# Kernel tuning notes

Hardware: AMD Instinct MI355X
Metric: run time of the kernel (lower is better)

## Reference

```python
import jax, jax.numpy as jnp
import numpy as np

B, A, E = 16384, 8, 512


def setup_inputs() -> dict:
    key = jax.random.key(0)
    ks = jax.random.split(key, 6)
    return {
        "image_features": jax.random.normal(ks[0], (B, E), dtype=jnp.float32),
        "edge_attributes": jax.random.normal(ks[1], (B, A, E), dtype=jnp.float32),
        "linear_w": jax.random.normal(ks[2], (E, 2 * E), dtype=jnp.float32) * (1.0 / np.sqrt(2 * E)),
        "linear_b": jax.random.normal(ks[3], (E,), dtype=jnp.float32) * 0.01,
        "fwd_proj": jax.random.normal(ks[4], (A, E, E), dtype=jnp.float32) * (1.0 / np.sqrt(E)),
        "bwd_proj": jax.random.normal(ks[5], (A, E, E), dtype=jnp.float32) * (1.0 / np.sqrt(E)),
        "self_weighted": jnp.ones((1, A, 1), dtype=jnp.float32),
    }


def reference(image_features, edge_attributes, linear_w, linear_b, fwd_proj, bwd_proj, self_weighted):
    # Forward attribute GNN: broadcast src over attribute axis, concat, linear(2E->E)
    src = jnp.broadcast_to(image_features[:, None, :], edge_attributes.shape)  # [B,A,E]
    x = jnp.concatenate([src, edge_attributes], axis=-1)                       # [B,A,2E]
    agg = jnp.einsum('bak,ek->bae', x, linear_w) + linear_b                    # [B,A,E]
    attr_rep = jnp.einsum('bai,aij->baj', agg, fwd_proj)                       # [B,A,E]

    # Backward attribute GNN: per-type projection, ReLU, learned weighted sum over A
    proj = jnp.einsum('bai,aij->baj', attr_rep, bwd_proj)                      # [B,A,E]
    individuals = jnp.sum(jax.nn.relu(proj) * self_weighted, axis=1)           # [B,E]
    return attr_rep, individuals
```

## Files before the change

kernel.cpp:

```cpp
#include <hip/hip_runtime.h>
#include <cstdint>
#include <cstddef>

#define NB 16384
#define NA 8
#define NE 512
#define NK 1024
#define NN 4096

typedef __bf16 bf16x8 __attribute__((ext_vector_type(8)));
typedef float  f32x4  __attribute__((ext_vector_type(4)));
typedef uint16_t u16x8 __attribute__((ext_vector_type(8)));

__device__ __forceinline__ uint16_t cvt_bf16(float f) {
    uint32_t u = __builtin_bit_cast(uint32_t, f);
    u += 0x7fffu + ((u >> 16) & 1u);
    return (uint16_t)(u >> 16);
}

__device__ __forceinline__ int swz(int row) { return (row ^ (row >> 2)) & 3; }

__device__ __forceinline__ int cf_pos(int row, int c) {
    return ((row >> 1) << 3) + ((((row & 1) << 2) + c) ^ ((row >> 1) & 7));
}

__device__ __forceinline__ void gl_lds16(const void* g, void* l) {
    __builtin_amdgcn_global_load_lds(
        (__attribute__((address_space(1))) void*)(void*)g,
        (__attribute__((address_space(3))) void*)l, 16, 0, 0);
}

__device__ __forceinline__ void tcvt_tile(const float* __restrict__ src,
                                          uint16_t* __restrict__ dst,
                                          int R, int C, int c0, int r0, int t) {
    __shared__ float tile[32][33];
    int tx = t & 31, ty = t >> 5;
#pragma unroll
    for (int yy = 0; yy < 4; ++yy) {
        int r = ty + yy * 8;
        tile[r][tx] = src[(size_t)(r0 + r) * C + c0 + tx];
    }
    __syncthreads();
#pragma unroll
    for (int yy = 0; yy < 4; ++yy) {
        int c = ty + yy * 8;
        dst[(size_t)(c0 + c) * R + r0 + tx] = cvt_bf16(tile[tx][c]);
    }
}

__global__ __launch_bounds__(256) void k_pre(const float* __restrict__ lw,
                                             const float* __restrict__ fwd,
                                             const float* __restrict__ bwd,
                                             const float* __restrict__ img,
                                             const float* __restrict__ lb,
                                             uint16_t* __restrict__ lwT,
                                             uint16_t* __restrict__ fwdT,
                                             uint16_t* __restrict__ bwdT,
                                             uint16_t* __restrict__ imgb,
                                             float* __restrict__ bvec) {
    int b = blockIdx.x, t = threadIdx.x;
    if (b < 512) {
        int bx = b & 31, by = b >> 5;
        tcvt_tile(lw, lwT, NE, NK, bx * 32, by * 32, t);
    } else if (b < 2560) {
        int i = b - 512;
        int mat = i >> 8, bx = i & 15, by = (i >> 4) & 15;
        tcvt_tile(fwd + (size_t)mat * NE * NE, fwdT + (size_t)mat * NE * NE,
                  NE, NE, bx * 32, by * 32, t);
    } else if (b < 4608) {
        int i = b - 2560;
        int mat = i >> 8, bx = i & 15, by = (i >> 4) & 15;
        tcvt_tile(bwd + (size_t)mat * NE * NE, bwdT + (size_t)mat * NE * NE,
                  NE, NE, bx * 32, by * 32, t);
    } else if (b < 12800) {
        int i = (b - 4608) * 256 + t;
        float4 v = ((const float4*)img)[i];
        ushort4 o;
        o.x = cvt_bf16(v.x); o.y = cvt_bf16(v.y); o.z = cvt_bf16(v.z); o.w = cvt_bf16(v.w);
        ((ushort4*)imgb)[i] = o;
    } else {
        int i = b - 12800;
        int a = i >> 4, i0 = (i & 15) * 32;
        float s0 = 0.f, s1 = 0.f;
#pragma unroll 4
        for (int k = 0; k < 32; ++k) {
            float w = lb[i0 + k];
            const float* f = fwd + ((size_t)a * NE + i0 + k) * NE;
            s0 = fmaf(w, f[t], s0);
            s1 = fmaf(w, f[t + 256], s1);
        }
        atomicAdd(&bvec[a * NE + t], s0);
        atomicAdd(&bvec[a * NE + t + 256], s1);
    }
}

__global__ __launch_bounds__(256) void k_prep(const uint16_t* __restrict__ lwT,
                                              const uint16_t* __restrict__ fwdT,
                                              uint16_t* __restrict__ TMT) {
    __shared__ alignas(16) uint16_t lA[128 * 32];
    __shared__ alignas(16) uint16_t lB[128 * 32];
    int bz = blockIdx.x;
    int nt = bz & 31, mt = bz >> 5;
    int m0 = mt * 128, n0 = nt * 128;
    int t = threadIdx.x, lane = t & 63;
    int w = t >> 6, wm = w >> 1, wn = w & 1;
    int lr = lane & 15, lc = lane >> 4;
    int sl = swz(lr);
    f32x4 acc[4][4] = {};
    for (int k0 = 0; k0 < NE; k0 += 32) {
        __syncthreads();
#pragma unroll
        for (int p = 0; p < 2; ++p) {
            int idx = p * 256 + t;
            int row = idx >> 2, c16 = (idx & 3) ^ swz(row);
            gl_lds16(lwT + (size_t)(m0 + row) * NE + k0 + c16 * 8, lA + idx * 8);
            gl_lds16(fwdT + (size_t)(n0 + row) * NE + k0 + c16 * 8, lB + idx * 8);
        }
        __syncthreads();
        bf16x8 af[4], bfr[4];
#pragma unroll
        for (int i = 0; i < 4; ++i)
            af[i] = *(const bf16x8*)&lA[(wm * 64 + i * 16 + lr) * 32 + ((lc ^ sl) << 3)];
#pragma unroll
        for (int j = 0; j < 4; ++j)
            bfr[j] = *(const bf16x8*)&lB[(wn * 64 + j * 16 + lr) * 32 + ((lc ^ sl) << 3)];
#pragma unroll
        for (int i = 0; i < 4; ++i)
#pragma unroll
            for (int j = 0; j < 4; ++j)
                acc[i][j] = __builtin_amdgcn_mfma_f32_16x16x32_bf16(af[i], bfr[j], acc[i][j], 0, 0, 0);
    }
#pragma unroll
    for (int i = 0; i < 4; ++i) {
        int mb = m0 + wm * 64 + i * 16 + lc * 4;
#pragma unroll
        for (int j = 0; j < 4; ++j) {
            int n = n0 + wn * 64 + j * 16 + lr;
            ushort4 v;
            v.x = cvt_bf16(acc[i][j][0]);
            v.y = cvt_bf16(acc[i][j][1]);
            v.z = cvt_bf16(acc[i][j][2]);
            v.w = cvt_bf16(acc[i][j][3]);
            *(ushort4*)&TMT[(size_t)n * NK + mb] = v;
        }
    }
}

__global__ __launch_bounds__(512) void k_mm4(const uint16_t* __restrict__ imgb,
                                             const float* __restrict__ edge,
                                             const uint16_t* __restrict__ TMT,
                                             const float* __restrict__ bvec,
                                             float* __restrict__ attr) {
    __shared__ alignas(16) uint16_t lA[2][128 * 32];
    __shared__ alignas(16) uint16_t lB[2][256 * 32];
    int o = blockIdx.x;
    int a = o & 7, idx = o >> 3;
    int jt = idx & 1, mt = idx >> 1;
    int m0 = mt * 128, jb = jt * 256;
    int t = threadIdx.x, lane = t & 63;
    int w = t >> 6, wm = w >> 2, wn = w & 3;
    int lr = lane & 15, lc = lane >> 4;
    int rpA = t >> 3, qA = (t & 7) ^ (rpA & 7);
    int srA = (rpA << 1) | (qA >> 2), scA = (qA & 3) << 3;
    int srB[2], scB[2];
#pragma unroll
    for (int p = 0; p < 2; ++p) {
        int u = t + p * 512;
        int rp = u >> 3, q = (u & 7) ^ (rp & 7);
        srB[p] = (rp << 1) | (q >> 2);
        scB[p] = (q & 3) << 3;
    }
    int er = t >> 2, ec = t & 3;
    int epos = cf_pos(er, ec) * 8;
    int aoff[4], boff[4];
#pragma unroll
    for (int i = 0; i < 4; ++i) {
        aoff[i] = cf_pos(wm * 64 + i * 16 + lr, lc) * 8;
        boff[i] = cf_pos(wn * 64 + i * 16 + lr, lc) * 8;
    }
    auto stage_img = [&](int buf, int s) {
        gl_lds16(imgb + (size_t)(m0 + srA) * NE + s * 32 + scA, &lA[buf][t * 8]);
    };
    auto stage_tmt = [&](int buf, int s) {
#pragma unroll
        for (int p = 0; p < 2; ++p)
            gl_lds16(TMT + (size_t)(a * NE + jb + srB[p]) * NK + s * 32 + scB[p],
                     &lB[buf][(t + p * 512) * 8]);
    };
    f32x4 acc[4][4] = {};
    stage_img(0, 0);
    stage_tmt(0, 0);
    for (int s = 0; s < 32; ++s) {
        int cur = s & 1, nb = cur ^ 1;
        __syncthreads();
        float4 e0, e1;
        bool eN = (s < 31) && (s + 1 >= 16);
        if (s < 31) {
            if (s + 1 < 16) {
                stage_img(nb, s + 1);
            } else {
                int kk = (s + 1 - 16) * 32;
                const float* sp = edge + ((size_t)(m0 + er) * NA + a) * NE + kk + ec * 8;
                e0 = ((const float4*)sp)[0];
                e1 = ((const float4*)sp)[1];
            }
            stage_tmt(nb, s + 1);
        }
        bf16x8 af[4], bfr[4];
#pragma unroll
        for (int i = 0; i < 4; ++i) af[i] = *(const bf16x8*)&lA[cur][aoff[i]];
#pragma unroll
        for (int j = 0; j < 4; ++j) bfr[j] = *(const bf16x8*)&lB[cur][boff[j]];
#pragma unroll
        for (int i = 0; i < 4; ++i)
#pragma unroll
            for (int j = 0; j < 4; ++j)
                acc[i][j] = __builtin_amdgcn_mfma_f32_16x16x32_bf16(af[i], bfr[j], acc[i][j], 0, 0, 0);
        if (eN) {
            u16x8 ov = {cvt_bf16(e0.x), cvt_bf16(e0.y), cvt_bf16(e0.z), cvt_bf16(e0.w),
                        cvt_bf16(e1.x), cvt_bf16(e1.y), cvt_bf16(e1.z), cvt_bf16(e1.w)};
            *(u16x8*)&lA[nb][epos] = ov;
        }
    }
#pragma unroll
    for (int j = 0; j < 4; ++j) {
        float bv = bvec[a * NE + jb + wn * 64 + j * 16 + lr];
#pragma unroll
        for (int i = 0; i < 4; ++i)
#pragma unroll
            for (int r = 0; r < 4; ++r)
                acc[i][j][r] += bv;
    }
#pragma unroll
    for (int i = 0; i < 4; ++i) {
#pragma unroll
        for (int r = 0; r < 4; ++r) {
            int bm = m0 + wm * 64 + i * 16 + lc * 4 + r;
            float* orow = attr + ((size_t)bm * NA + a) * NE + jb;
#pragma unroll
            for (int j = 0; j < 4; ++j)
                orow[wn * 64 + j * 16 + lr] = acc[i][j][r];
        }
    }
}

__global__ __launch_bounds__(256) void k_ind4(const float* __restrict__ attrf,
                                              const uint16_t* __restrict__ bwdT,
                                              const float* __restrict__ sw,
                                              float* __restrict__ ind) {
    __shared__ alignas(16) uint16_t lA[2][128 * 32];
    __shared__ alignas(16) uint16_t lB[2][128 * 32];
    int o = blockIdx.x;
    int xcd = o & 7, mt = o >> 3;
    int jt = xcd >> 1, ah = xcd & 1;
    int m0 = mt * 128, jb = jt * 128, a0 = ah * 4;
    int t = threadIdx.x, lane = t & 63;
    int w = t >> 6, wm = w >> 1, wn = w & 1;
    int lr = lane & 15, lc = lane >> 4;
    int srow[2], sc8[2];
#pragma unroll
    for (int p = 0; p < 2; ++p) {
        int u = p * 256 + t;
        int rp = u >> 3, q = (u & 7) ^ (rp & 7);
        srow[p] = (rp << 1) | (q >> 2);
        sc8[p] = (q & 3) << 3;
    }
    int erow[2], ec[2], epos[2];
#pragma unroll
    for (int p = 0; p < 2; ++p) {
        int u = p * 256 + t;
        erow[p] = u >> 2; ec[p] = u & 3;
        epos[p] = cf_pos(erow[p], ec[p]) * 8;
    }
    int aoff[4], boff[4];
#pragma unroll
    for (int i = 0; i < 4; ++i) {
        aoff[i] = cf_pos(wm * 64 + i * 16 + lr, lc) * 8;
        boff[i] = cf_pos(wn * 64 + i * 16 + lr, lc) * 8;
    }
    auto stage = [&](int buf, int s) {
        int aa = a0 + (s >> 4), kk = (s & 15) * 32;
#pragma unroll
        for (int p = 0; p < 2; ++p) {
            const float* sp = attrf + ((size_t)(m0 + erow[p]) * NA + aa) * NE + kk + ec[p] * 8;
            float4 v0 = ((const float4*)sp)[0];
            float4 v1 = ((const float4*)sp)[1];
            u16x8 ov = {cvt_bf16(v0.x), cvt_bf16(v0.y), cvt_bf16(v0.z), cvt_bf16(v0.w),
                        cvt_bf16(v1.x), cvt_bf16(v1.y), cvt_bf16(v1.z), cvt_bf16(v1.w)};
            *(u16x8*)&lA[buf][epos[p]] = ov;
        }
#pragma unroll
        for (int p = 0; p < 2; ++p)
            gl_lds16(bwdT + (size_t)(aa * NE + jb + srow[p]) * NE + kk + sc8[p],
                     &lB[buf][(p * 256 + t) * 8]);
    };
    f32x4 res[4][4] = {};
    f32x4 acc[4][4] = {};
    stage(0, 0);
    for (int s = 0; s < 64; ++s) {
        int cur = s & 1;
        __syncthreads();
        if (s < 63) stage(cur ^ 1, s + 1);
        bf16x8 af[4], bfr[4];
#pragma unroll
        for (int i = 0; i < 4; ++i) af[i] = *(const bf16x8*)&lA[cur][aoff[i]];
#pragma unroll
        for (int j = 0; j < 4; ++j) bfr[j] = *(const bf16x8*)&lB[cur][boff[j]];
#pragma unroll
        for (int i = 0; i < 4; ++i)
#pragma unroll
            for (int j = 0; j < 4; ++j)
                acc[i][j] = __builtin_amdgcn_mfma_f32_16x16x32_bf16(af[i], bfr[j], acc[i][j], 0, 0, 0);
        if ((s & 15) == 15) {
            float wa = sw[a0 + (s >> 4)];
#pragma unroll
            for (int i = 0; i < 4; ++i)
#pragma unroll
                for (int j = 0; j < 4; ++j) {
#pragma unroll
                    for (int r = 0; r < 4; ++r)
                        res[i][j][r] += wa * fmaxf(acc[i][j][r], 0.f);
                    acc[i][j] = (f32x4){0.f, 0.f, 0.f, 0.f};
                }
        }
    }
#pragma unroll
    for (int i = 0; i < 4; ++i) {
#pragma unroll
        for (int r = 0; r < 4; ++r) {
            int bm = m0 + wm * 64 + i * 16 + lc * 4 + r;
            float* orow = ind + (size_t)bm * NE + jb;
#pragma unroll
            for (int j = 0; j < 4; ++j)
                atomicAdd(&orow[wn * 64 + j * 16 + lr], res[i][j][r]);
        }
    }
}

extern "C" void kernel_launch(void* const* d_in, const int* in_sizes, int n_in,
                              void* d_out, int out_size, void* d_ws, size_t ws_size,
                              hipStream_t stream) {
    (void)in_sizes; (void)n_in; (void)out_size; (void)ws_size;
    const float* img  = (const float*)d_in[0];
    const float* edge = (const float*)d_in[1];
    const float* lw   = (const float*)d_in[2];
    const float* lb   = (const float*)d_in[3];
    const float* fwd  = (const float*)d_in[4];
    const float* bwd  = (const float*)d_in[5];
    const float* sw   = (const float*)d_in[6];
    float* attr = (float*)d_out;
    float* ind  = attr + (size_t)NB * NA * NE;

    char* ws = (char*)d_ws;
    size_t off = 0;
    auto alloc = [&](size_t bytes) { void* p = ws + off; off += bytes; return p; };
    uint16_t* lwT  = (uint16_t*)alloc((size_t)NK * NE * 2);
    uint16_t* fwdT = (uint16_t*)alloc((size_t)NA * NE * NE * 2);
    uint16_t* bwdT = (uint16_t*)alloc((size_t)NA * NE * NE * 2);
    uint16_t* TMT  = (uint16_t*)alloc((size_t)NN * NK * 2);
    uint16_t* imgb = (uint16_t*)alloc((size_t)NB * NE * 2);
    float*    bvec = (float*)alloc((size_t)NN * 4);

    hipMemsetAsync(bvec, 0, (size_t)NN * 4, stream);
    hipMemsetAsync(ind, 0, (size_t)NB * NE * 4, stream);

    k_pre<<<12928, 256, 0, stream>>>(lw, fwd, bwd, img, lb, lwT, fwdT, bwdT, imgb, bvec);
    k_prep<<<(NK / 128) * (NN / 128), 256, 0, stream>>>(lwT, fwdT, TMT);

    int mm_grid = 8 * 2 * (NB / 128);
    int ind_grid = (NB / 128) * (NE / 128) * 2;

    k_mm4<<<mm_grid, 512, 0, stream>>>(imgb, edge, TMT, bvec, attr);
    k_ind4<<<ind_grid, 256, 0, stream>>>(attr, bwdT, sw, ind);
}
```

Before: 500.3 us.

## Emit bf16 copy of attr_rep and enlarge individuals kernel tiles to 128x256

```diff
diff --git a/kernel.cpp b/kernel.cpp
--- a/kernel.cpp
+++ b/kernel.cpp
@@ -146,11 +146,13 @@
     }
 }
 
+template<bool WB>
 __global__ __launch_bounds__(512) void k_mm4(const uint16_t* __restrict__ imgb,
                                              const float* __restrict__ edge,
                                              const uint16_t* __restrict__ TMT,
                                              const float* __restrict__ bvec,
-                                             float* __restrict__ attr) {
+                                             float* __restrict__ attr,
+                                             uint16_t* __restrict__ attrb) {
     __shared__ alignas(16) uint16_t lA[2][128 * 32];
     __shared__ alignas(16) uint16_t lB[2][256 * 32];
     int o = blockIdx.x;
@@ -240,38 +242,42 @@
 #pragma unroll
             for (int j = 0; j < 4; ++j)
                 orow[wn * 64 + j * 16 + lr] = acc[i][j][r];
-        }
-    }
-}
-
-__global__ __launch_bounds__(256) void k_ind4(const float* __restrict__ attrf,
+            if (WB) {
+                uint16_t* brw = attrb + ((size_t)bm * NA + a) * NE + jb;
+#pragma unroll
+                for (int j = 0; j < 4; ++j)
+                    brw[wn * 64 + j * 16 + lr] = cvt_bf16(acc[i][j][r]);
+            }
+        }
+    }
+}
+
+template<bool AB>
+__global__ __launch_bounds__(512) void k_ind5(const float* __restrict__ attrf,
+                                              const uint16_t* __restrict__ attrb,
                                               const uint16_t* __restrict__ bwdT,
                                               const float* __restrict__ sw,
                                               float* __restrict__ ind) {
     __shared__ alignas(16) uint16_t lA[2][128 * 32];
-    __shared__ alignas(16) uint16_t lB[2][128 * 32];
+    __shared__ alignas(16) uint16_t lB[2][256 * 32];
     int o = blockIdx.x;
-    int xcd = o & 7, mt = o >> 3;
-    int jt = xcd >> 1, ah = xcd & 1;
-    int m0 = mt * 128, jb = jt * 128, a0 = ah * 4;
+    int ah = o & 1, jt = (o >> 1) & 1, mt = o >> 2;
+    int m0 = mt * 128, jb = jt * 256, a0 = ah * 4;
     int t = threadIdx.x, lane = t & 63;
-    int w = t >> 6, wm = w >> 1, wn = w & 1;
+    int w = t >> 6, wm = w >> 2, wn = w & 3;
     int lr = lane & 15, lc = lane >> 4;
-    int srow[2], sc8[2];
+    int rpA = t >> 3, qA = (t & 7) ^ (rpA & 7);
+    int srA = (rpA << 1) | (qA >> 2), scA = (qA & 3) << 3;
+    int srB[2], scB[2];
 #pragma unroll
     for (int p = 0; p < 2; ++p) {
-        int u = p * 256 + t;
+        int u = t + p * 512;
         int rp = u >> 3, q = (u & 7) ^ (rp & 7);
-        srow[p] = (rp << 1) | (q >> 2);
-        sc8[p] = (q & 3) << 3;
-    }
-    int erow[2], ec[2], epos[2];
-#pragma unroll
-    for (int p = 0; p < 2; ++p) {
-        int u = p * 256 + t;
-        erow[p] = u >> 2; ec[p] = u & 3;
-        epos[p] = cf_pos(erow[p], ec[p]) * 8;
-    }
+        srB[p] = (rp << 1) | (q >> 2);
+        scB[p] = (q & 3) << 3;
+    }
+    int er = t >> 2, ec = t & 3;
+    int epos = cf_pos(er, ec) * 8;
     int aoff[4], boff[4];
 #pragma unroll
     for (int i = 0; i < 4; ++i) {
@@ -280,19 +286,21 @@
     }
     auto stage = [&](int buf, int s) {
         int aa = a0 + (s >> 4), kk = (s & 15) * 32;
-#pragma unroll
-        for (int p = 0; p < 2; ++p) {
-            const float* sp = attrf + ((size_t)(m0 + erow[p]) * NA + aa) * NE + kk + ec[p] * 8;
+        if (AB) {
+            gl_lds16(attrb + ((size_t)(m0 + srA) * NA + aa) * NE + kk + scA,
+                     &lA[buf][t * 8]);
+        } else {
+            const float* sp = attrf + ((size_t)(m0 + er) * NA + aa) * NE + kk + ec * 8;
             float4 v0 = ((const float4*)sp)[0];
             float4 v1 = ((const float4*)sp)[1];
             u16x8 ov = {cvt_bf16(v0.x), cvt_bf16(v0.y), cvt_bf16(v0.z), cvt_bf16(v0.w),
                         cvt_bf16(v1.x), cvt_bf16(v1.y), cvt_bf16(v1.z), cvt_bf16(v1.w)};
-            *(u16x8*)&lA[buf][epos[p]] = ov;
+            *(u16x8*)&lA[buf][epos] = ov;
         }
 #pragma unroll
         for (int p = 0; p < 2; ++p)
-            gl_lds16(bwdT + (size_t)(aa * NE + jb + srow[p]) * NE + kk + sc8[p],
-                     &lB[buf][(p * 256 + t) * 8]);
+            gl_lds16(bwdT + (size_t)(aa * NE + jb + srB[p]) * NE + kk + scB[p],
+                     &lB[buf][(t + p * 512) * 8]);
     };
     f32x4 res[4][4] = {};
     f32x4 acc[4][4] = {};
@@ -340,7 +348,7 @@
 extern "C" void kernel_launch(void* const* d_in, const int* in_sizes, int n_in,
                               void* d_out, int out_size, void* d_ws, size_t ws_size,
                               hipStream_t stream) {
-    (void)in_sizes; (void)n_in; (void)out_size; (void)ws_size;
+    (void)in_sizes; (void)n_in; (void)out_size;
     const float* img  = (const float*)d_in[0];
     const float* edge = (const float*)d_in[1];
     const float* lw   = (const float*)d_in[2];
@@ -361,6 +369,10 @@
     uint16_t* imgb = (uint16_t*)alloc((size_t)NB * NE * 2);
     float*    bvec = (float*)alloc((size_t)NN * 4);
 
+    const size_t BIGB = (size_t)NB * NA * NE * 2;
+    bool has_attrb = ws_size >= off + BIGB;
+    uint16_t* attrb = has_attrb ? (uint16_t*)alloc(BIGB) : (uint16_t*)0;
+
     hipMemsetAsync(bvec, 0, (size_t)NN * 4, stream);
     hipMemsetAsync(ind, 0, (size_t)NB * NE * 4, stream);
 
@@ -368,8 +380,13 @@
     k_prep<<<(NK / 128) * (NN / 128), 256, 0, stream>>>(lwT, fwdT, TMT);
 
     int mm_grid = 8 * 2 * (NB / 128);
-    int ind_grid = (NB / 128) * (NE / 128) * 2;
-
-    k_mm4<<<mm_grid, 512, 0, stream>>>(imgb, edge, TMT, bvec, attr);
-    k_ind4<<<ind_grid, 256, 0, stream>>>(attr, bwdT, sw, ind);
-}
+    int ind_grid = (NB / 128) * 2 * 2;
+
+    if (has_attrb) {
+        k_mm4<true><<<mm_grid, 512, 0, stream>>>(imgb, edge, TMT, bvec, attr, attrb);
+        k_ind5<true><<<ind_grid, 512, 0, stream>>>(attr, attrb, bwdT, sw, ind);
+    } else {
+        k_mm4<false><<<mm_grid, 512, 0, stream>>>(imgb, edge, TMT, bvec, attr, attrb);
+        k_ind5<false><<<ind_grid, 512, 0, stream>>>(attr, attrb, bwdT, sw, ind);
+    }
+}
```

New measurement: 477.8 us. 4.5% less time.

## Deepen k_mm pipeline with manual waitcnt and emit bf16 attr copy for k_ind

Applied to the files above, without the earlier changes.

```diff
diff --git a/kernel.cpp b/kernel.cpp
--- a/kernel.cpp
+++ b/kernel.cpp
@@ -146,11 +146,13 @@
     }
 }
 
-__global__ __launch_bounds__(512) void k_mm4(const uint16_t* __restrict__ imgb,
+template<bool WB>
+__global__ __launch_bounds__(512) void k_mm6(const uint16_t* __restrict__ imgb,
                                              const float* __restrict__ edge,
                                              const uint16_t* __restrict__ TMT,
                                              const float* __restrict__ bvec,
-                                             float* __restrict__ attr) {
+                                             float* __restrict__ attr,
+                                             uint16_t* __restrict__ attrb) {
     __shared__ alignas(16) uint16_t lA[2][128 * 32];
     __shared__ alignas(16) uint16_t lB[2][256 * 32];
     int o = blockIdx.x;
@@ -178,50 +180,80 @@
         aoff[i] = cf_pos(wm * 64 + i * 16 + lr, lc) * 8;
         boff[i] = cf_pos(wn * 64 + i * 16 + lr, lc) * 8;
     }
-    auto stage_img = [&](int buf, int s) {
-        gl_lds16(imgb + (size_t)(m0 + srA) * NE + s * 32 + scA, &lA[buf][t * 8]);
-    };
-    auto stage_tmt = [&](int buf, int s) {
-#pragma unroll
-        for (int p = 0; p < 2; ++p)
-            gl_lds16(TMT + (size_t)(a * NE + jb + srB[p]) * NK + s * 32 + scB[p],
-                     &lB[buf][(t + p * 512) * 8]);
-    };
+    const uint16_t* gA  = imgb + (size_t)(m0 + srA) * NE + scA;
+    const uint16_t* gB0 = TMT + (size_t)(a * NE + jb + srB[0]) * NK + scB[0];
+    const uint16_t* gB1 = TMT + (size_t)(a * NE + jb + srB[1]) * NK + scB[1];
+    const float*    gE  = edge + ((size_t)(m0 + er) * NA + a) * NE + ec * 8;
+
     f32x4 acc[4][4] = {};
-    stage_img(0, 0);
-    stage_tmt(0, 0);
-    for (int s = 0; s < 32; ++s) {
-        int cur = s & 1, nb = cur ^ 1;
-        __syncthreads();
-        float4 e0, e1;
-        bool eN = (s < 31) && (s + 1 >= 16);
-        if (s < 31) {
-            if (s + 1 < 16) {
-                stage_img(nb, s + 1);
-            } else {
-                int kk = (s + 1 - 16) * 32;
-                const float* sp = edge + ((size_t)(m0 + er) * NA + a) * NE + kk + ec * 8;
-                e0 = ((const float4*)sp)[0];
-                e1 = ((const float4*)sp)[1];
-            }
-            stage_tmt(nb, s + 1);
-        }
-        bf16x8 af[4], bfr[4];
-#pragma unroll
-        for (int i = 0; i < 4; ++i) af[i] = *(const bf16x8*)&lA[cur][aoff[i]];
-#pragma unroll
-        for (int j = 0; j < 4; ++j) bfr[j] = *(const bf16x8*)&lB[cur][boff[j]];
-#pragma unroll
-        for (int i = 0; i < 4; ++i)
-#pragma unroll
-            for (int j = 0; j < 4; ++j)
-                acc[i][j] = __builtin_amdgcn_mfma_f32_16x16x32_bf16(af[i], bfr[j], acc[i][j], 0, 0, 0);
-        if (eN) {
-            u16x8 ov = {cvt_bf16(e0.x), cvt_bf16(e0.y), cvt_bf16(e0.z), cvt_bf16(e0.w),
-                        cvt_bf16(e1.x), cvt_bf16(e1.y), cvt_bf16(e1.z), cvt_bf16(e1.w)};
-            *(u16x8*)&lA[nb][epos] = ov;
-        }
-    }
+    float4 e[2][2];
+
+#define FRAGS_AND_MFMA(CUR)                                                        \
+    {                                                                              \
+        bf16x8 af[4], bfr[4];                                                      \
+        _Pragma("unroll")                                                          \
+        for (int i = 0; i < 4; ++i) af[i] = *(const bf16x8*)&lA[CUR][aoff[i]];     \
+        _Pragma("unroll")                                                          \
+        for (int j = 0; j < 4; ++j) bfr[j] = *(const bf16x8*)&lB[CUR][boff[j]];    \
+        asm volatile("s_waitcnt lgkmcnt(0)" ::: "memory");                         \
+        __builtin_amdgcn_sched_barrier(0);                                         \
+        _Pragma("unroll")                                                          \
+        for (int i = 0; i < 4; ++i)                                                \
+            _Pragma("unroll")                                                      \
+            for (int j = 0; j < 4; ++j)                                            \
+                acc[i][j] = __builtin_amdgcn_mfma_f32_16x16x32_bf16(af[i], bfr[j], acc[i][j], 0, 0, 0); \
+    }
+
+    gl_lds16(gA,       &lA[0][t * 8]);
+    gl_lds16(gB0,      &lB[0][t * 8]);
+    gl_lds16(gB1,      &lB[0][(t + 512) * 8]);
+    gl_lds16(gA + 32,  &lA[1][t * 8]);
+    gl_lds16(gB0 + 32, &lB[1][t * 8]);
+    gl_lds16(gB1 + 32, &lB[1][(t + 512) * 8]);
+
+#pragma unroll 2
+    for (int s = 0; s < 14; ++s) {
+        int cur = s & 1;
+        asm volatile("s_waitcnt vmcnt(3) lgkmcnt(0)\n\ts_barrier" ::: "memory");
+        if (s == 13) {
+            e[0][0] = *(const float4*)gE;
+            e[0][1] = *(const float4*)(gE + 4);
+        }
+        FRAGS_AND_MFMA(cur);
+        asm volatile("s_barrier" ::: "memory");
+        gl_lds16(gA + (s + 2) * 32,  &lA[cur][t * 8]);
+        gl_lds16(gB0 + (s + 2) * 32, &lB[cur][t * 8]);
+        gl_lds16(gB1 + (s + 2) * 32, &lB[cur][(t + 512) * 8]);
+    }
+
+#pragma unroll 2
+    for (int s = 14; s < 30; ++s) {
+        int cur = s & 1;
+        asm volatile("s_waitcnt vmcnt(3) lgkmcnt(0)\n\ts_barrier" ::: "memory");
+        if (s < 29) {
+            float4* eo = e[(s + 1) & 1];
+            eo[0] = *(const float4*)(gE + (s - 13) * 32);
+            eo[1] = *(const float4*)(gE + (s - 13) * 32 + 4);
+        }
+        FRAGS_AND_MFMA(cur);
+        asm volatile("s_barrier" ::: "memory");
+        {
+            const float4* ei = e[s & 1];
+            u16x8 ov = {cvt_bf16(ei[0].x), cvt_bf16(ei[0].y), cvt_bf16(ei[0].z), cvt_bf16(ei[0].w),
+                        cvt_bf16(ei[1].x), cvt_bf16(ei[1].y), cvt_bf16(ei[1].z), cvt_bf16(ei[1].w)};
+            *(u16x8*)&lA[cur][epos] = ov;
+        }
+        gl_lds16(gB0 + (s + 2) * 32, &lB[cur][t * 8]);
+        gl_lds16(gB1 + (s + 2) * 32, &lB[cur][(t + 512) * 8]);
+    }
+
+    asm volatile("s_waitcnt vmcnt(2) lgkmcnt(0)\n\ts_barrier" ::: "memory");
+    FRAGS_AND_MFMA(0);
+    asm volatile("s_barrier" ::: "memory");
+    asm volatile("s_waitcnt vmcnt(0) lgkmcnt(0)\n\ts_barrier" ::: "memory");
+    FRAGS_AND_MFMA(1);
+#undef FRAGS_AND_MFMA
+
 #pragma unroll
     for (int j = 0; j < 4; ++j) {
         float bv = bvec[a * NE + jb + wn * 64 + j * 16 + lr];
@@ -240,11 +272,19 @@
 #pragma unroll
             for (int j = 0; j < 4; ++j)
                 orow[wn * 64 + j * 16 + lr] = acc[i][j][r];
-        }
-    }
-}
-
+            if (WB) {
+                uint16_t* brw = attrb + ((size_t)bm * NA + a) * NE + jb;
+#pragma unroll
+                for (int j = 0; j < 4; ++j)
+                    brw[wn * 64 + j * 16 + lr] = cvt_bf16(acc[i][j][r]);
+            }
+        }
+    }
+}
+
+template<bool AB>
 __global__ __launch_bounds__(256) void k_ind4(const float* __restrict__ attrf,
+                                              const uint16_t* __restrict__ attrb,
                                               const uint16_t* __restrict__ bwdT,
                                               const float* __restrict__ sw,
                                               float* __restrict__ ind) {
@@ -280,14 +320,21 @@
     }
     auto stage = [&](int buf, int s) {
         int aa = a0 + (s >> 4), kk = (s & 15) * 32;
-#pragma unroll
-        for (int p = 0; p < 2; ++p) {
-            const float* sp = attrf + ((size_t)(m0 + erow[p]) * NA + aa) * NE + kk + ec[p] * 8;
-            float4 v0 = ((const float4*)sp)[0];
-            float4 v1 = ((const float4*)sp)[1];
-            u16x8 ov = {cvt_bf16(v0.x), cvt_bf16(v0.y), cvt_bf16(v0.z), cvt_bf16(v0.w),
-                        cvt_bf16(v1.x), cvt_bf16(v1.y), cvt_bf16(v1.z), cvt_bf16(v1.w)};
-            *(u16x8*)&lA[buf][epos[p]] = ov;
+        if (AB) {
+#pragma unroll
+            for (int p = 0; p < 2; ++p)
+                gl_lds16(attrb + ((size_t)(m0 + srow[p]) * NA + aa) * NE + kk + sc8[p],
+                         &lA[buf][(p * 256 + t) * 8]);
+        } else {
+#pragma unroll
+            for (int p = 0; p < 2; ++p) {
+                const float* sp = attrf + ((size_t)(m0 + erow[p]) * NA + aa) * NE + kk + ec[p] * 8;
+                float4 v0 = ((const float4*)sp)[0];
+                float4 v1 = ((const float4*)sp)[1];
+                u16x8 ov = {cvt_bf16(v0.x), cvt_bf16(v0.y), cvt_bf16(v0.z), cvt_bf16(v0.w),
+                            cvt_bf16(v1.x), cvt_bf16(v1.y), cvt_bf16(v1.z), cvt_bf16(v1.w)};
+                *(u16x8*)&lA[buf][epos[p]] = ov;
+            }
         }
 #pragma unroll
         for (int p = 0; p < 2; ++p)
@@ -340,7 +387,7 @@
 extern "C" void kernel_launch(void* const* d_in, const int* in_sizes, int n_in,
                               void* d_out, int out_size, void* d_ws, size_t ws_size,
                               hipStream_t stream) {
-    (void)in_sizes; (void)n_in; (void)out_size; (void)ws_size;
+    (void)in_sizes; (void)n_in; (void)out_size;
     const float* img  = (const float*)d_in[0];
     const float* edge = (const float*)d_in[1];
     const float* lw   = (const float*)d_in[2];
@@ -361,6 +408,10 @@
     uint16_t* imgb = (uint16_t*)alloc((size_t)NB * NE * 2);
     float*    bvec = (float*)alloc((size_t)NN * 4);
 
+    const size_t BIGB = (size_t)NB * NA * NE * 2;
+    bool has_attrb = ws_size >= off + BIGB;
+    uint16_t* attrb = has_attrb ? (uint16_t*)alloc(BIGB) : (uint16_t*)0;
+
     hipMemsetAsync(bvec, 0, (size_t)NN * 4, stream);
     hipMemsetAsync(ind, 0, (size_t)NB * NE * 4, stream);
 
@@ -370,6 +421,11 @@
     int mm_grid = 8 * 2 * (NB / 128);
     int ind_grid = (NB / 128) * (NE / 128) * 2;
 
-    k_mm4<<<mm_grid, 512, 0, stream>>>(imgb, edge, TMT, bvec, attr);
-    k_ind4<<<ind_grid, 256, 0, stream>>>(attr, bwdT, sw, ind);
-}
+    if (has_attrb) {
+        k_mm6<true><<<mm_grid, 512, 0, stream>>>(imgb, edge, TMT, bvec, attr, attrb);
+        k_ind4<true><<<ind_grid, 256, 0, stream>>>(attr, attrb, bwdT, sw, ind);
+    } else {
+        k_mm6<false><<<mm_grid, 512, 0, stream>>>(imgb, edge, TMT, bvec, attr, attrb);
+        k_ind4<false><<<ind_grid, 256, 0, stream>>>(attr, attrb, bwdT, sw, ind);
+    }
+}
```

After: 476.9 us. 4.7% less time.
